# Kernel optimization log

Hardware: AMD Instinct MI355X
Metric: run time of the kernel (lower is better)

## Reference

```python
import jax, jax.numpy as jnp
import numpy as np

B, T, M, P = 512, 64, 256, 256


def setup_inputs() -> dict:
    key = jax.random.key(0)
    ks = jax.random.split(key, 17)
    w = lambda i, shape: (jax.random.normal(ks[i], shape, jnp.float32) * 0.05)
    return {
        "encoded_inputs": jax.random.normal(ks[0], (B, T, M), jnp.float32),
        "y": jax.random.normal(ks[1], (B, T, 1), jnp.float32),
        "tar": jax.random.normal(ks[2], (B, 2), jnp.float32),
        "train": 1,
        "Wd_w": w(3, (M, 2 * P)), "Wd_b": w(4, (M,)),
        "Ud_w": w(5, (M, M)),
        "vd_w": w(6, (1, M)),
        "wt_w": w(7, (1, M + 1)), "wt_b": w(8, (1,)),
        "Wy_w": w(9, (P, P + M)), "Wy_b": w(10, (P,)),
        "vy_w": w(11, (1, P)), "vy_b": w(12, (1,)),
        "Wih": w(13, (4 * P, 1)), "Whh": w(14, (4 * P, P)),
        "bih": w(15, (4 * P,)), "bhh": w(16, (4 * P,)),
    }


def _lstm_cell(x, h, c, Wih, Whh, bih, bhh):
    # torch.nn.LSTMCell gate order: i, f, g, o
    g = x @ Wih.T + h @ Whh.T + (bih + bhh)
    i, f, gg, o = jnp.split(g, 4, axis=1)
    c = jax.nn.sigmoid(f) * c + jax.nn.sigmoid(i) * jnp.tanh(gg)
    h = jax.nn.sigmoid(o) * jnp.tanh(c)
    return h, c


def reference(encoded_inputs, y, tar, train,
              Wd_w, Wd_b, Ud_w, vd_w, wt_w, wt_b,
              Wy_w, Wy_b, vy_w, vy_b, Wih, Whh, bih, bhh):
    Bn = encoded_inputs.shape[0]
    Pn = Whh.shape[1]
    Mn = encoded_inputs.shape[2]
    h0 = jnp.zeros((Bn, Pn), encoded_inputs.dtype)
    c0 = jnp.zeros((Bn, Pn), encoded_inputs.dtype)
    ctx0 = jnp.zeros((Bn, Mn), encoded_inputs.dtype)
    # U_d(encoded_inputs) is loop-invariant
    y1 = jnp.einsum('btm,nm->btn', encoded_inputs, Ud_w)  # (B,T,M)

    def attend(h, s):
        x1 = jnp.concatenate([h, s], axis=1) @ Wd_w.T + Wd_b      # (B,M)
        z1 = jnp.tanh(x1[:, None, :] + y1)                        # (B,T,M)
        l = jnp.einsum('btm,m->bt', z1, vd_w[0])                  # (B,T)
        beta = jax.nn.softmax(l, axis=1)
        return jnp.einsum('bt,btm->bm', beta, encoded_inputs)     # (B,M)

    def step(carry, y_t):
        h, s, _ = carry
        c_t = attend(h, s)
        y_til = jnp.concatenate([c_t, y_t], axis=1) @ wt_w.T + wt_b  # (B,1)
        h, s = _lstm_cell(y_til, h, s, Wih, Whh, bih, bhh)
        return (h, s, c_t), None

    (h, s, c_t), _ = jax.lax.scan(step, (h0, c0, ctx0), jnp.swapaxes(y, 0, 1))

    def head(h):
        return (jnp.concatenate([h, c_t], axis=1) @ Wy_w.T + Wy_b) @ vy_w.T + vy_b

    def extra(h, s, inp):
        y_til = jnp.concatenate([c_t, inp], axis=1) @ wt_w.T + wt_b
        h, s = _lstm_cell(y_til, h, s, Wih, Whh, bih, bhh)
        return h, s, head(h)

    y_Tp1 = head(h)
    if train:
        h, s, y_Tp2 = extra(h, s, tar[:, 0:1])
        h, s, y_Tp3 = extra(h, s, tar[:, 1:2])
    else:
        h, s, y_Tp2 = extra(h, s, y_Tp1)
        h, s, y_Tp3 = extra(h, s, y_Tp2)
    return (y_Tp1, y_Tp2, y_Tp3)
```

## Files before the change

kernel.cpp:

```cpp
#include <hip/hip_runtime.h>


typedef unsigned short u16;
typedef unsigned int u32;
typedef _Float16 half_t;
typedef half_t h2 __attribute__((ext_vector_type(2)));

#define BB 512
#define TT 64
#define MM 256
#define PP 256
#define YS 264
#define ES 68

#define WD16_OFF  0
#define WHH16_OFF 131072
#define WY16_OFF  393216
#define WQ_ELEMS  524288
#define WQ_BYTES  (WQ_ELEMS * 2)

struct H8 { h2 p[4]; };

#if defined(__has_builtin)
#if __has_builtin(__builtin_amdgcn_fdot2)
#define FDOT2(a, b, c) __builtin_amdgcn_fdot2((a), (b), (c), false)
#endif
#endif
#ifndef FDOT2
__device__ __forceinline__ float FDOT2(h2 a, h2 b, float c) {
  return c + (float)a[0] * (float)b[0] + (float)a[1] * (float)b[1];
}
#endif

__device__ __forceinline__ float dot8(const H8 w, const H8 a, float acc) {
  acc = FDOT2(w.p[0], a.p[0], acc);
  acc = FDOT2(w.p[1], a.p[1], acc);
  acc = FDOT2(w.p[2], a.p[2], acc);
  acc = FDOT2(w.p[3], a.p[3], acc);
  return acc;
}
__device__ __forceinline__ u16 f2h(float f) {
  union { half_t h; u16 u; } x; x.h = (half_t)f; return x.u;
}
__device__ __forceinline__ void unpackH8(const H8 v, float f[8]) {
#pragma unroll
  for (int i = 0; i < 8; ++i) f[i] = (float)v.p[i >> 1][i & 1];
}
__device__ __forceinline__ void ldf8(const float* p, float f[8]) {
  float4 a = *(const float4*)p;
  float4 b = *(const float4*)(p + 4);
  f[0]=a.x; f[1]=a.y; f[2]=a.z; f[3]=a.w;
  f[4]=b.x; f[5]=b.y; f[6]=b.z; f[7]=b.w;
}
__device__ __forceinline__ float tanh_fast(float x) {
  float e = __builtin_amdgcn_exp2f(x * 2.885390081777927f);
  return 1.0f - 2.0f * __builtin_amdgcn_rcpf(1.0f + e);
}
__device__ __forceinline__ float sigmoid_fast(float x) {
  float e = __builtin_amdgcn_exp2f(x * -1.4426950408889634f);
  return __builtin_amdgcn_rcpf(1.0f + e);
}

__global__ __launch_bounds__(256) void prep_kernel(
    const float* __restrict__ Wd, const float* __restrict__ Whh,
    const float* __restrict__ Wy, u16* __restrict__ o) {
  int i = blockIdx.x * 256 + threadIdx.x;
  float v;
  if (i < WHH16_OFF) {
    int ki = i & 7, n = (i >> 3) & 255, kb = i >> 11;
    v = Wd[n * 512 + kb * 8 + ki];
  } else if (i < WY16_OFF) {
    int r = i - WHH16_OFF;
    int ki = r & 7, n = (r >> 3) & 1023, kb = r >> 13;
    v = Whh[n * 256 + kb * 8 + ki];
  } else {
    int r = i - WY16_OFF;
    int ki = r & 7, n = (r >> 3) & 255, kb = r >> 11;
    v = Wy[n * 512 + kb * 8 + ki];
  }
  o[i] = f2h(v);
}

template <int WQ>
__global__ __launch_bounds__(256, 2) void scan_kernel(
    const float* __restrict__ E,
    const float* __restrict__ yin,
    const float* __restrict__ tar,
    const int*   __restrict__ train,
    const void*  __restrict__ Wd_q,
    const float* __restrict__ Wd_b,
    const float* __restrict__ Ud_w,
    const float* __restrict__ vd_w,
    const float* __restrict__ wt_w,
    const float* __restrict__ wt_b,
    const void*  __restrict__ Wy_q,
    const float* __restrict__ Wy_b,
    const float* __restrict__ vy_w,
    const float* __restrict__ vy_b,
    const float* __restrict__ Wih,
    const void*  __restrict__ Whh_q,
    const float* __restrict__ bih,
    const float* __restrict__ bhh,
    float* __restrict__ out)
{
  __shared__ __align__(16) u16   y1l[TT * YS];
  __shared__ __align__(16) u16   e16T[MM * ES];
  __shared__ __align__(16) u32   hs16[256];
  __shared__ __align__(16) u32   ctx16p[128];
  __shared__ __align__(16) float ctx[MM];
  __shared__ __align__(16) float x1s[MM];
  __shared__ __align__(16) float lpart[4][TT];
  __shared__ __align__(16) u16   betas16[TT];
  __shared__ float red[4];
  __shared__ float sc[2];

  const int j = threadIdx.x;
  const int b = blockIdx.x;
  const int wv = j >> 6;

  hs16[j] = 0;
  float creg = 0.f;

  {
    const float* __restrict__ Eb = E + (size_t)b * TT * MM;
    for (int i = j; i < TT * MM; i += 256) {
      int t = i >> 8, m = i & 255;
      e16T[m * ES + t] = f2h(Eb[i]);
    }
  }

  {
    const float* __restrict__ Eb = E + (size_t)b * TT * MM;
    const float* __restrict__ Uj = Ud_w + (size_t)j * MM;
    for (int t0 = 0; t0 < TT; t0 += 16) {
      float acc[16];
#pragma unroll
      for (int i = 0; i < 16; ++i) acc[i] = 0.f;
      for (int m0 = 0; m0 < MM; m0 += 8) {
        float w[8]; ldf8(Uj + m0, w);
#pragma unroll
        for (int tt = 0; tt < 16; ++tt) {
          float e[8]; ldf8(Eb + (size_t)(t0 + tt) * MM + m0, e);
#pragma unroll
          for (int mm = 0; mm < 8; ++mm) acc[tt] = fmaf(e[mm], w[mm], acc[tt]);
        }
      }
#pragma unroll
      for (int tt = 0; tt < 16; ++tt)
        y1l[(t0 + tt) * YS + j] = f2h(acc[tt]);
    }
  }
  __syncthreads();

  auto mv4 = [&](float& g0, float& g1, float& g2, float& g3) {
    g0 = g1 = g2 = g3 = 0.f;
    if (WQ) {
      const u16* W = (const u16*)Whh_q;
      const u16* p0 = W + (size_t)j * 8;
      const u16* p1 = p0 + 256 * 8;
      const u16* p2 = p0 + 512 * 8;
      const u16* p3 = p0 + 768 * 8;
#pragma unroll 4
      for (int kb = 0; kb < 32; ++kb) {
        H8 hp = *(const H8*)&hs16[kb * 4];
        g0 = dot8(*(const H8*)p0, hp, g0); p0 += 8192;
        g1 = dot8(*(const H8*)p1, hp, g1); p1 += 8192;
        g2 = dot8(*(const H8*)p2, hp, g2); p2 += 8192;
        g3 = dot8(*(const H8*)p3, hp, g3); p3 += 8192;
      }
    } else {
      const float* W = (const float*)Whh_q;
      const float* p0 = W + (size_t)j * 256;
#pragma unroll 2
      for (int kb = 0; kb < 32; ++kb) {
        H8 hp = *(const H8*)&hs16[kb * 4];
        float hf[8]; unpackH8(hp, hf);
        float w0[8], w1[8], w2[8], w3[8];
        ldf8(p0 + kb * 8, w0);
        ldf8(p0 + 256 * 256 + kb * 8, w1);
        ldf8(p0 + 512 * 256 + kb * 8, w2);
        ldf8(p0 + 768 * 256 + kb * 8, w3);
#pragma unroll
        for (int i = 0; i < 8; ++i) {
          g0 = fmaf(hf[i], w0[i], g0);
          g1 = fmaf(hf[i], w1[i], g1);
          g2 = fmaf(hf[i], w2[i], g2);
          g3 = fmaf(hf[i], w3[i], g3);
        }
      }
    }
  };

  auto gates_apply = [&](float g0, float g1, float g2, float g3, float ytil) {
    g0 += ytil * Wih[j]       + bih[j]       + bhh[j];
    g1 += ytil * Wih[j + 256] + bih[j + 256] + bhh[j + 256];
    g2 += ytil * Wih[j + 512] + bih[j + 512] + bhh[j + 512];
    g3 += ytil * Wih[j + 768] + bih[j + 768] + bhh[j + 768];
    float c = sigmoid_fast(g1) * creg + sigmoid_fast(g0) * tanh_fast(g2);
    float h = sigmoid_fast(g3) * tanh_fast(c);
    creg = c;
    u16* hsu = (u16*)hs16;
    hsu[j] = f2h(h);
    hsu[256 + j] = f2h(c);
  };

  auto head_store = [&](int outIdx) {
    float p = 0.f;
    if (WQ) {
      const u16* W = (const u16*)Wy_q;
      const u16* ph = W + (size_t)j * 8;
      const u16* pc = W + (size_t)(32 * 256 + j) * 8;
#pragma unroll 4
      for (int kb = 0; kb < 32; ++kb) {
        H8 hp = *(const H8*)&hs16[kb * 4];
        H8 cp = *(const H8*)&ctx16p[kb * 4];
        p = dot8(*(const H8*)ph, hp, p); ph += 2048;
        p = dot8(*(const H8*)pc, cp, p); pc += 2048;
      }
    } else {
      const float* W = (const float*)Wy_q + (size_t)j * 512;
      for (int kb = 0; kb < 32; ++kb) {
        H8 hp = *(const H8*)&hs16[kb * 4];
        float hf[8]; unpackH8(hp, hf);
        float w0[8], w1[8];
        ldf8(W + kb * 8, w0);
        ldf8(W + 256 + kb * 8, w1);
#pragma unroll
        for (int i = 0; i < 8; ++i) {
          p = fmaf(hf[i], w0[i], p);
          p = fmaf(ctx[kb * 8 + i], w1[i], p);
        }
      }
    }
    float pp = (p + Wy_b[j]) * vy_w[j];
#pragma unroll
    for (int off = 32; off; off >>= 1) pp += __shfl_xor(pp, off, 64);
    if ((j & 63) == 0) red[wv] = pp;
    __syncthreads();
    if (j == 0) {
      float o = red[0] + red[1] + red[2] + red[3] + vy_b[0];
      out[(size_t)outIdx * BB + b] = o;
      sc[0] = o;
    }
    __syncthreads();
  };

  for (int step = 0; step < TT; ++step) {
    float ax0 = 0.f, ax1 = 0.f, g0, g1, g2, g3;
    {
      if (WQ) {
        const u16* Wd16 = (const u16*)Wd_q;
        const u16* Wh16 = (const u16*)Whh_q;
        const u16* pdh = Wd16 + (size_t)j * 8;
        const u16* pdc = Wd16 + (size_t)(32 * 256 + j) * 8;
        const u16* p0 = Wh16 + (size_t)j * 8;
        const u16* p1 = p0 + 256 * 8;
        const u16* p2 = p0 + 512 * 8;
        const u16* p3 = p0 + 768 * 8;
        float b0 = 0.f, b1 = 0.f, b2 = 0.f, b3 = 0.f;
#pragma unroll 4
        for (int kb = 0; kb < 32; ++kb) {
          H8 hp = *(const H8*)&hs16[kb * 4];
          H8 cp = *(const H8*)&hs16[128 + kb * 4];
          ax0 = dot8(*(const H8*)pdh, hp, ax0); pdh += 2048;
          ax1 = dot8(*(const H8*)pdc, cp, ax1); pdc += 2048;
          b0 = dot8(*(const H8*)p0, hp, b0); p0 += 8192;
          b1 = dot8(*(const H8*)p1, hp, b1); p1 += 8192;
          b2 = dot8(*(const H8*)p2, hp, b2); p2 += 8192;
          b3 = dot8(*(const H8*)p3, hp, b3); p3 += 8192;
        }
        g0 = b0; g1 = b1; g2 = b2; g3 = b3;
      } else {
        const float* wd = (const float*)Wd_q + (size_t)j * 512;
        const float* w0p = (const float*)Whh_q + (size_t)j * 256;
        float b0 = 0.f, b1 = 0.f, b2 = 0.f, b3 = 0.f;
#pragma unroll 2
        for (int kb = 0; kb < 32; ++kb) {
          H8 hp = *(const H8*)&hs16[kb * 4];
          H8 cp = *(const H8*)&hs16[128 + kb * 4];
          float hf[8], cf[8]; unpackH8(hp, hf); unpackH8(cp, cf);
          float wh[8], wc[8], w0[8], w1[8], w2[8], w3[8];
          ldf8(wd + kb * 8, wh);
          ldf8(wd + 256 + kb * 8, wc);
          ldf8(w0p + kb * 8, w0);
          ldf8(w0p + 256 * 256 + kb * 8, w1);
          ldf8(w0p + 512 * 256 + kb * 8, w2);
          ldf8(w0p + 768 * 256 + kb * 8, w3);
#pragma unroll
          for (int i = 0; i < 8; ++i) {
            ax0 = fmaf(hf[i], wh[i], ax0);
            ax1 = fmaf(cf[i], wc[i], ax1);
            b0 = fmaf(hf[i], w0[i], b0);
            b1 = fmaf(hf[i], w1[i], b1);
            b2 = fmaf(hf[i], w2[i], b2);
            b3 = fmaf(hf[i], w3[i], b3);
          }
        }
        g0 = b0; g1 = b1; g2 = b2; g3 = b3;
      }
      x1s[j] = ax0 + ax1 + Wd_b[j];
    }
    __syncthreads();

    {
      const int q = wv, tq = j & 63;
      const u16* __restrict__ yrow = &y1l[tq * YS + q * 64];
      const float* __restrict__ xp = &x1s[q * 64];
      const float* __restrict__ vp = vd_w + q * 64;
      float lp = 0.f;
#pragma unroll 2
      for (int m0 = 0; m0 < 64; m0 += 8) {
        H8 yv = *(const H8*)(yrow + m0);
        float yf[8]; unpackH8(yv, yf);
        float xf[8]; ldf8(xp + m0, xf);
        float vf[8]; ldf8(vp + m0, vf);
#pragma unroll
        for (int mm = 0; mm < 8; ++mm) {
          float z = tanh_fast(xf[mm] + yf[mm]);
          lp = fmaf(z, vf[mm], lp);
        }
      }
      lpart[q][tq] = lp;
    }
    __syncthreads();

    if (j < 64) {
      const int t = j;
      float l = lpart[0][t] + lpart[1][t] + lpart[2][t] + lpart[3][t];
      float mx = l;
#pragma unroll
      for (int off = 32; off; off >>= 1) mx = fmaxf(mx, __shfl_xor(mx, off, 64));
      float e = __builtin_amdgcn_exp2f((l - mx) * 1.4426950408889634f);
      float sm = e;
#pragma unroll
      for (int off = 32; off; off >>= 1) sm += __shfl_xor(sm, off, 64);
      betas16[t] = f2h(e * __builtin_amdgcn_rcpf(sm));
    }
    __syncthreads();

    {
      const u16* __restrict__ ep = &e16T[j * ES];
      float acc = 0.f;
#pragma unroll
      for (int t0 = 0; t0 < TT; t0 += 8) {
        h2 e0 = *(const h2*)(ep + t0);
        h2 e1 = *(const h2*)(ep + t0 + 2);
        h2 e2 = *(const h2*)(ep + t0 + 4);
        h2 e3 = *(const h2*)(ep + t0 + 6);
        H8 bp = *(const H8*)&betas16[t0];
        acc = FDOT2(bp.p[0], e0, acc);
        acc = FDOT2(bp.p[1], e1, acc);
        acc = FDOT2(bp.p[2], e2, acc);
        acc = FDOT2(bp.p[3], e3, acc);
      }
      ctx[j] = acc;
      ((u16*)ctx16p)[j] = f2h(acc);
    }
    {
      float p = ctx[j] * wt_w[j];
#pragma unroll
      for (int off = 32; off; off >>= 1) p += __shfl_xor(p, off, 64);
      if ((j & 63) == 0) red[wv] = p;
    }
    __syncthreads();
    {
      float ytil = red[0] + red[1] + red[2] + red[3]
                 + yin[(size_t)b * TT + step] * wt_w[MM] + wt_b[0];
      gates_apply(g0, g1, g2, g3, ytil);
    }
    __syncthreads();
  }

  float ctdot;
  {
    float p = ctx[j] * wt_w[j];
#pragma unroll
    for (int off = 32; off; off >>= 1) p += __shfl_xor(p, off, 64);
    if ((j & 63) == 0) red[wv] = p;
    __syncthreads();
    ctdot = red[0] + red[1] + red[2] + red[3];
    __syncthreads();
  }

  head_store(0);

  const int tr = train[0];
  for (int e = 0; e < 2; ++e) {
    float inp = tr ? tar[(size_t)b * 2 + e] : sc[0];
    float ytil = ctdot + inp * wt_w[MM] + wt_b[0];
    float g0, g1, g2, g3;
    mv4(g0, g1, g2, g3);
    gates_apply(g0, g1, g2, g3, ytil);
    __syncthreads();
    head_store(1 + e);
  }
}

extern "C" void kernel_launch(void* const* d_in, const int* in_sizes, int n_in,
                              void* d_out, int out_size, void* d_ws, size_t ws_size,
                              hipStream_t stream) {
  const float* E     = (const float*)d_in[0];
  const float* yin   = (const float*)d_in[1];
  const float* tar   = (const float*)d_in[2];
  const int*   train = (const int*)d_in[3];
  const float* Wd_w  = (const float*)d_in[4];
  const float* Wd_b  = (const float*)d_in[5];
  const float* Ud_w  = (const float*)d_in[6];
  const float* vd_w  = (const float*)d_in[7];
  const float* wt_w  = (const float*)d_in[8];
  const float* wt_b  = (const float*)d_in[9];
  const float* Wy_w  = (const float*)d_in[10];
  const float* Wy_b  = (const float*)d_in[11];
  const float* vy_w  = (const float*)d_in[12];
  const float* vy_b  = (const float*)d_in[13];
  const float* Wih   = (const float*)d_in[14];
  const float* Whh   = (const float*)d_in[15];
  const float* bih   = (const float*)d_in[16];
  const float* bhh   = (const float*)d_in[17];

  float* out = (float*)d_out;

  if (ws_size >= (size_t)WQ_BYTES) {
    u16* wq = (u16*)d_ws;
    prep_kernel<<<dim3(WQ_ELEMS / 256), dim3(256), 0, stream>>>(
        Wd_w, Whh, Wy_w, wq);
    scan_kernel<1><<<dim3(BB), dim3(256), 0, stream>>>(
        E, yin, tar, train, wq + WD16_OFF, Wd_b, Ud_w, vd_w, wt_w, wt_b,
        wq + WY16_OFF, Wy_b, vy_w, vy_b, Wih, wq + WHH16_OFF, bih, bhh, out);
  } else {
    scan_kernel<0><<<dim3(BB), dim3(256), 0, stream>>>(
        E, yin, tar, train, Wd_w, Wd_b, Ud_w, vd_w, wt_w, wt_b,
        Wy_w, Wy_b, vy_w, vy_b, Wih, Whh, bih, bhh, out);
  }

  (void)in_sizes; (void)n_in; (void)out_size;
}
```

Measured before the change: 1.192 ms.

## Process two batch rows per block with split-K matvecs sharing weight loads

Each block now handles two batch rows with 512 threads. The two thread halves split the K dimension of the recurrent and attention matvecs, and each weight vector load is reused for both rows, with partial sums combined through shared memory. The intent is to halve per-row weight traffic from global/L2 and double the work per block. The cost is doubled LDS use per block (two copies of y1 and E^T), which likely limits occupancy to one block per CU, plus extra reduction syncs.

```diff
diff --git a/kernel.cpp b/kernel.cpp
--- a/kernel.cpp
+++ b/kernel.cpp
@@ -12,6 +12,8 @@
 #define PP 256
 #define YS 264
 #define ES 68
+#define NROW 2
+#define NTH 512
 
 #define WD16_OFF  0
 #define WHH16_OFF 131072
@@ -82,7 +84,7 @@
 }
 
 template <int WQ>
-__global__ __launch_bounds__(256, 2) void scan_kernel(
+__global__ __launch_bounds__(NTH, 2) void scan_kernel(
     const float* __restrict__ E,
     const float* __restrict__ yin,
     const float* __restrict__ tar,
@@ -103,35 +105,49 @@
     const float* __restrict__ bhh,
     float* __restrict__ out)
 {
-  __shared__ __align__(16) u16   y1l[TT * YS];
-  __shared__ __align__(16) u16   e16T[MM * ES];
-  __shared__ __align__(16) u32   hs16[256];
-  __shared__ __align__(16) u32   ctx16p[128];
-  __shared__ __align__(16) float ctx[MM];
-  __shared__ __align__(16) float x1s[MM];
-  __shared__ __align__(16) float lpart[4][TT];
-  __shared__ __align__(16) u16   betas16[TT];
-  __shared__ float red[4];
-  __shared__ float sc[2];
-
-  const int j = threadIdx.x;
-  const int b = blockIdx.x;
+  __shared__ __align__(16) u16   y1l[NROW][TT * YS];
+  __shared__ __align__(16) u16   e16T[NROW][MM * ES];
+  __shared__ __align__(16) u32   hs16[NROW][256];
+  __shared__ __align__(16) u32   ctx16p[NROW][128];
+  __shared__ __align__(16) float ctx[NROW][MM];
+  __shared__ __align__(16) float x1a[NROW][MM];
+  __shared__ __align__(16) float x1b[NROW][MM];
+  __shared__ __align__(16) float lpart[NROW][4][TT];
+  __shared__ __align__(16) u16   betas16[NROW][TT];
+  __shared__ __align__(16) float part[10][MM];
+  __shared__ float red[8];
+  __shared__ float sc[NROW];
+
+  const int j  = threadIdx.x;
+  const int n  = j & 255;
+  const int kh = j >> 8;
   const int wv = j >> 6;
-
-  hs16[j] = 0;
-  float creg = 0.f;
+  const int b0 = blockIdx.x * NROW;
+
+  ((u32*)hs16)[j] = 0;
+  float creg0 = 0.f, creg1 = 0.f;
+
+  const float wih0 = Wih[n],       wih1 = Wih[n + 256];
+  const float wih2 = Wih[n + 512], wih3 = Wih[n + 768];
+  const float bb0 = bih[n]       + bhh[n];
+  const float bb1 = bih[n + 256] + bhh[n + 256];
+  const float bb2 = bih[n + 512] + bhh[n + 512];
+  const float bb3 = bih[n + 768] + bhh[n + 768];
+  const float wtM = wt_w[MM], wtb = wt_b[0];
 
   {
-    const float* __restrict__ Eb = E + (size_t)b * TT * MM;
-    for (int i = j; i < TT * MM; i += 256) {
-      int t = i >> 8, m = i & 255;
-      e16T[m * ES + t] = f2h(Eb[i]);
+    const float* __restrict__ Eb0 = E + (size_t)b0 * TT * MM;
+    for (int i = j; i < NROW * TT * MM; i += NTH) {
+      int r = i >> 14;
+      int idx = i & 16383;
+      int t = idx >> 8, m = idx & 255;
+      e16T[r][m * ES + t] = f2h(Eb0[i]);
     }
   }
 
   {
-    const float* __restrict__ Eb = E + (size_t)b * TT * MM;
-    const float* __restrict__ Uj = Ud_w + (size_t)j * MM;
+    const float* __restrict__ Eb = E + (size_t)(b0 + kh) * TT * MM;
+    const float* __restrict__ Uj = Ud_w + (size_t)n * MM;
     for (int t0 = 0; t0 < TT; t0 += 16) {
       float acc[16];
 #pragma unroll
@@ -147,186 +163,202 @@
       }
 #pragma unroll
       for (int tt = 0; tt < 16; ++tt)
-        y1l[(t0 + tt) * YS + j] = f2h(acc[tt]);
+        y1l[kh][(t0 + tt) * YS + n] = f2h(acc[tt]);
     }
   }
   __syncthreads();
 
-  auto mv4 = [&](float& g0, float& g1, float& g2, float& g3) {
-    g0 = g1 = g2 = g3 = 0.f;
+  auto gates_apply = [&](int r, float g0, float g1, float g2, float g3,
+                         float ytil) {
+    g0 += ytil * wih0 + bb0;
+    g1 += ytil * wih1 + bb1;
+    g2 += ytil * wih2 + bb2;
+    g3 += ytil * wih3 + bb3;
+    float& cr = r ? creg1 : creg0;
+    float c = sigmoid_fast(g1) * cr + sigmoid_fast(g0) * tanh_fast(g2);
+    float h = sigmoid_fast(g3) * tanh_fast(c);
+    cr = c;
+    u16* hsu = (u16*)hs16[r];
+    hsu[n] = f2h(h);
+    hsu[256 + n] = f2h(c);
+  };
+
+  auto head_store = [&](int outIdx) {
+    float p0 = 0.f, p1 = 0.f;
     if (WQ) {
-      const u16* W = (const u16*)Whh_q;
-      const u16* p0 = W + (size_t)j * 8;
-      const u16* p1 = p0 + 256 * 8;
-      const u16* p2 = p0 + 512 * 8;
-      const u16* p3 = p0 + 768 * 8;
+      const u16* Wy16 = (const u16*)Wy_q;
+      const u16* ph = Wy16 + (size_t)((kh * 16) * 256 + n) * 8;
+      const u16* pc = Wy16 + (size_t)((32 + kh * 16) * 256 + n) * 8;
+      const u32* hb0 = &hs16[0][kh * 64];
+      const u32* hb1 = &hs16[1][kh * 64];
+      const u32* cb0 = &ctx16p[0][kh * 64];
+      const u32* cb1 = &ctx16p[1][kh * 64];
 #pragma unroll 4
-      for (int kb = 0; kb < 32; ++kb) {
-        H8 hp = *(const H8*)&hs16[kb * 4];
-        g0 = dot8(*(const H8*)p0, hp, g0); p0 += 8192;
-        g1 = dot8(*(const H8*)p1, hp, g1); p1 += 8192;
-        g2 = dot8(*(const H8*)p2, hp, g2); p2 += 8192;
-        g3 = dot8(*(const H8*)p3, hp, g3); p3 += 8192;
+      for (int kb2 = 0; kb2 < 16; ++kb2) {
+        H8 wh = *(const H8*)ph; ph += 2048;
+        H8 wc = *(const H8*)pc; pc += 2048;
+        H8 hp0 = *(const H8*)&hb0[kb2 * 4];
+        H8 hp1 = *(const H8*)&hb1[kb2 * 4];
+        H8 cp0 = *(const H8*)&cb0[kb2 * 4];
+        H8 cp1 = *(const H8*)&cb1[kb2 * 4];
+        p0 = dot8(wh, hp0, p0); p0 = dot8(wc, cp0, p0);
+        p1 = dot8(wh, hp1, p1); p1 = dot8(wc, cp1, p1);
       }
     } else {
-      const float* W = (const float*)Whh_q;
-      const float* p0 = W + (size_t)j * 256;
+      const float* W = (const float*)Wy_q + (size_t)n * 512 + kh * 128;
 #pragma unroll 2
-      for (int kb = 0; kb < 32; ++kb) {
-        H8 hp = *(const H8*)&hs16[kb * 4];
-        float hf[8]; unpackH8(hp, hf);
-        float w0[8], w1[8], w2[8], w3[8];
-        ldf8(p0 + kb * 8, w0);
-        ldf8(p0 + 256 * 256 + kb * 8, w1);
-        ldf8(p0 + 512 * 256 + kb * 8, w2);
-        ldf8(p0 + 768 * 256 + kb * 8, w3);
+      for (int kb2 = 0; kb2 < 16; ++kb2) {
+        H8 hp0v = *(const H8*)&hs16[0][kh * 64 + kb2 * 4];
+        H8 hp1v = *(const H8*)&hs16[1][kh * 64 + kb2 * 4];
+        float hf0[8], hf1[8]; unpackH8(hp0v, hf0); unpackH8(hp1v, hf1);
+        float ch0[8], ch1[8];
+        ldf8(&ctx[0][kh * 128 + kb2 * 8], ch0);
+        ldf8(&ctx[1][kh * 128 + kb2 * 8], ch1);
+        float wh[8], wc[8];
+        ldf8(W + kb2 * 8, wh);
+        ldf8(W + 256 + kb2 * 8, wc);
 #pragma unroll
         for (int i = 0; i < 8; ++i) {
-          g0 = fmaf(hf[i], w0[i], g0);
-          g1 = fmaf(hf[i], w1[i], g1);
-          g2 = fmaf(hf[i], w2[i], g2);
-          g3 = fmaf(hf[i], w3[i], g3);
+          p0 = fmaf(hf0[i], wh[i], p0); p0 = fmaf(ch0[i], wc[i], p0);
+          p1 = fmaf(hf1[i], wh[i], p1); p1 = fmaf(ch1[i], wc[i], p1);
         }
       }
     }
+    if (kh) { part[0][n] = p0; part[1][n] = p1; }
+    __syncthreads();
+    if (kh == 0) {
+      float q0 = (p0 + part[0][n] + Wy_b[n]) * vy_w[n];
+      float q1 = (p1 + part[1][n] + Wy_b[n]) * vy_w[n];
+#pragma unroll
+      for (int off = 32; off; off >>= 1) {
+        q0 += __shfl_xor(q0, off, 64);
+        q1 += __shfl_xor(q1, off, 64);
+      }
+      if ((j & 63) == 0) { red[wv] = q0; red[4 + wv] = q1; }
+    }
+    __syncthreads();
+    if (j == 0) {
+      float o0 = red[0] + red[1] + red[2] + red[3] + vy_b[0];
+      float o1 = red[4] + red[5] + red[6] + red[7] + vy_b[0];
+      out[(size_t)outIdx * BB + b0] = o0;
+      out[(size_t)outIdx * BB + b0 + 1] = o1;
+      sc[0] = o0; sc[1] = o1;
+    }
+    __syncthreads();
   };
 
-  auto gates_apply = [&](float g0, float g1, float g2, float g3, float ytil) {
-    g0 += ytil * Wih[j]       + bih[j]       + bhh[j];
-    g1 += ytil * Wih[j + 256] + bih[j + 256] + bhh[j + 256];
-    g2 += ytil * Wih[j + 512] + bih[j + 512] + bhh[j + 512];
-    g3 += ytil * Wih[j + 768] + bih[j + 768] + bhh[j + 768];
-    float c = sigmoid_fast(g1) * creg + sigmoid_fast(g0) * tanh_fast(g2);
-    float h = sigmoid_fast(g3) * tanh_fast(c);
-    creg = c;
-    u16* hsu = (u16*)hs16;
-    hsu[j] = f2h(h);
-    hsu[256 + j] = f2h(c);
-  };
-
-  auto head_store = [&](int outIdx) {
-    float p = 0.f;
-    if (WQ) {
-      const u16* W = (const u16*)Wy_q;
-      const u16* ph = W + (size_t)j * 8;
-      const u16* pc = W + (size_t)(32 * 256 + j) * 8;
-#pragma unroll 4
-      for (int kb = 0; kb < 32; ++kb) {
-        H8 hp = *(const H8*)&hs16[kb * 4];
-        H8 cp = *(const H8*)&ctx16p[kb * 4];
-        p = dot8(*(const H8*)ph, hp, p); ph += 2048;
-        p = dot8(*(const H8*)pc, cp, p); pc += 2048;
-      }
-    } else {
-      const float* W = (const float*)Wy_q + (size_t)j * 512;
-      for (int kb = 0; kb < 32; ++kb) {
-        H8 hp = *(const H8*)&hs16[kb * 4];
-        float hf[8]; unpackH8(hp, hf);
-        float w0[8], w1[8];
-        ldf8(W + kb * 8, w0);
-        ldf8(W + 256 + kb * 8, w1);
-#pragma unroll
-        for (int i = 0; i < 8; ++i) {
-          p = fmaf(hf[i], w0[i], p);
-          p = fmaf(ctx[kb * 8 + i], w1[i], p);
-        }
-      }
-    }
-    float pp = (p + Wy_b[j]) * vy_w[j];
-#pragma unroll
-    for (int off = 32; off; off >>= 1) pp += __shfl_xor(pp, off, 64);
-    if ((j & 63) == 0) red[wv] = pp;
-    __syncthreads();
-    if (j == 0) {
-      float o = red[0] + red[1] + red[2] + red[3] + vy_b[0];
-      out[(size_t)outIdx * BB + b] = o;
-      sc[0] = o;
-    }
-    __syncthreads();
-  };
-
   for (int step = 0; step < TT; ++step) {
-    float ax0 = 0.f, ax1 = 0.f, g0, g1, g2, g3;
+    float sg0r0 = 0, sg0r1 = 0, sg1r0 = 0, sg1r1 = 0;
+    float sg2r0 = 0, sg2r1 = 0, sg3r0 = 0, sg3r1 = 0;
     {
+      float ax0 = 0.f, ax1 = 0.f;
+      float g00 = 0, g01 = 0, g10 = 0, g11 = 0;
+      float g20 = 0, g21 = 0, g30 = 0, g31 = 0;
       if (WQ) {
         const u16* Wd16 = (const u16*)Wd_q;
         const u16* Wh16 = (const u16*)Whh_q;
-        const u16* pdh = Wd16 + (size_t)j * 8;
-        const u16* pdc = Wd16 + (size_t)(32 * 256 + j) * 8;
-        const u16* p0 = Wh16 + (size_t)j * 8;
+        const u16* pdh = Wd16 + (size_t)((kh * 16) * 256 + n) * 8;
+        const u16* pdc = Wd16 + (size_t)((32 + kh * 16) * 256 + n) * 8;
+        const u16* p0 = Wh16 + (size_t)((kh * 16) * 1024 + n) * 8;
         const u16* p1 = p0 + 256 * 8;
         const u16* p2 = p0 + 512 * 8;
         const u16* p3 = p0 + 768 * 8;
-        float b0 = 0.f, b1 = 0.f, b2 = 0.f, b3 = 0.f;
+        const u32* hb0 = &hs16[0][kh * 64];
+        const u32* hb1 = &hs16[1][kh * 64];
+        const u32* cb0 = &hs16[0][128 + kh * 64];
+        const u32* cb1 = &hs16[1][128 + kh * 64];
 #pragma unroll 4
-        for (int kb = 0; kb < 32; ++kb) {
-          H8 hp = *(const H8*)&hs16[kb * 4];
-          H8 cp = *(const H8*)&hs16[128 + kb * 4];
-          ax0 = dot8(*(const H8*)pdh, hp, ax0); pdh += 2048;
-          ax1 = dot8(*(const H8*)pdc, cp, ax1); pdc += 2048;
-          b0 = dot8(*(const H8*)p0, hp, b0); p0 += 8192;
-          b1 = dot8(*(const H8*)p1, hp, b1); p1 += 8192;
-          b2 = dot8(*(const H8*)p2, hp, b2); p2 += 8192;
-          b3 = dot8(*(const H8*)p3, hp, b3); p3 += 8192;
+        for (int kb2 = 0; kb2 < 16; ++kb2) {
+          H8 hp0 = *(const H8*)&hb0[kb2 * 4];
+          H8 hp1 = *(const H8*)&hb1[kb2 * 4];
+          H8 cp0 = *(const H8*)&cb0[kb2 * 4];
+          H8 cp1 = *(const H8*)&cb1[kb2 * 4];
+          H8 wdh = *(const H8*)pdh; pdh += 2048;
+          H8 wdc = *(const H8*)pdc; pdc += 2048;
+          H8 w0 = *(const H8*)p0; p0 += 8192;
+          H8 w1 = *(const H8*)p1; p1 += 8192;
+          H8 w2 = *(const H8*)p2; p2 += 8192;
+          H8 w3 = *(const H8*)p3; p3 += 8192;
+          ax0 = dot8(wdh, hp0, ax0); ax0 = dot8(wdc, cp0, ax0);
+          ax1 = dot8(wdh, hp1, ax1); ax1 = dot8(wdc, cp1, ax1);
+          g00 = dot8(w0, hp0, g00); g01 = dot8(w0, hp1, g01);
+          g10 = dot8(w1, hp0, g10); g11 = dot8(w1, hp1, g11);
+          g20 = dot8(w2, hp0, g20); g21 = dot8(w2, hp1, g21);
+          g30 = dot8(w3, hp0, g30); g31 = dot8(w3, hp1, g31);
         }
-        g0 = b0; g1 = b1; g2 = b2; g3 = b3;
       } else {
-        const float* wd = (const float*)Wd_q + (size_t)j * 512;
-        const float* w0p = (const float*)Whh_q + (size_t)j * 256;
-        float b0 = 0.f, b1 = 0.f, b2 = 0.f, b3 = 0.f;
+        const float* wdp = (const float*)Wd_q + (size_t)n * 512 + kh * 128;
+        const float* w0p = (const float*)Whh_q + (size_t)n * 256 + kh * 128;
 #pragma unroll 2
-        for (int kb = 0; kb < 32; ++kb) {
-          H8 hp = *(const H8*)&hs16[kb * 4];
-          H8 cp = *(const H8*)&hs16[128 + kb * 4];
-          float hf[8], cf[8]; unpackH8(hp, hf); unpackH8(cp, cf);
+        for (int kb2 = 0; kb2 < 16; ++kb2) {
+          H8 hp0v = *(const H8*)&hs16[0][kh * 64 + kb2 * 4];
+          H8 hp1v = *(const H8*)&hs16[1][kh * 64 + kb2 * 4];
+          H8 cp0v = *(const H8*)&hs16[0][128 + kh * 64 + kb2 * 4];
+          H8 cp1v = *(const H8*)&hs16[1][128 + kh * 64 + kb2 * 4];
+          float hf0[8], hf1[8], cf0[8], cf1[8];
+          unpackH8(hp0v, hf0); unpackH8(hp1v, hf1);
+          unpackH8(cp0v, cf0); unpackH8(cp1v, cf1);
           float wh[8], wc[8], w0[8], w1[8], w2[8], w3[8];
-          ldf8(wd + kb * 8, wh);
-          ldf8(wd + 256 + kb * 8, wc);
-          ldf8(w0p + kb * 8, w0);
-          ldf8(w0p + 256 * 256 + kb * 8, w1);
-          ldf8(w0p + 512 * 256 + kb * 8, w2);
-          ldf8(w0p + 768 * 256 + kb * 8, w3);
+          ldf8(wdp + kb2 * 8, wh);
+          ldf8(wdp + 256 + kb2 * 8, wc);
+          ldf8(w0p + kb2 * 8, w0);
+          ldf8(w0p + 256 * 256 + kb2 * 8, w1);
+          ldf8(w0p + 512 * 256 + kb2 * 8, w2);
+          ldf8(w0p + 768 * 256 + kb2 * 8, w3);
 #pragma unroll
           for (int i = 0; i < 8; ++i) {
-            ax0 = fmaf(hf[i], wh[i], ax0);
-            ax1 = fmaf(cf[i], wc[i], ax1);
-            b0 = fmaf(hf[i], w0[i], b0);
-            b1 = fmaf(hf[i], w1[i], b1);
-            b2 = fmaf(hf[i], w2[i], b2);
-            b3 = fmaf(hf[i], w3[i], b3);
+            ax0 = fmaf(hf0[i], wh[i], ax0); ax0 = fmaf(cf0[i], wc[i], ax0);
+            ax1 = fmaf(hf1[i], wh[i], ax1); ax1 = fmaf(cf1[i], wc[i], ax1);
+            g00 = fmaf(hf0[i], w0[i], g00); g01 = fmaf(hf1[i], w0[i], g01);
+            g10 = fmaf(hf0[i], w1[i], g10); g11 = fmaf(hf1[i], w1[i], g11);
+            g20 = fmaf(hf0[i], w2[i], g20); g21 = fmaf(hf1[i], w2[i], g21);
+            g30 = fmaf(hf0[i], w3[i], g30); g31 = fmaf(hf1[i], w3[i], g31);
           }
         }
-        g0 = b0; g1 = b1; g2 = b2; g3 = b3;
-      }
-      x1s[j] = ax0 + ax1 + Wd_b[j];
+      }
+      if (kh) {
+        x1b[0][n] = ax0; x1b[1][n] = ax1;
+        part[2][n] = g00; part[3][n] = g01;
+        part[4][n] = g10; part[5][n] = g11;
+        part[6][n] = g20; part[7][n] = g21;
+        part[8][n] = g30; part[9][n] = g31;
+      } else {
+        float bia = Wd_b[n];
+        x1a[0][n] = ax0 + bia; x1a[1][n] = ax1 + bia;
+        sg0r0 = g00; sg0r1 = g01; sg1r0 = g10; sg1r1 = g11;
+        sg2r0 = g20; sg2r1 = g21; sg3r0 = g30; sg3r1 = g31;
+      }
     }
     __syncthreads();
 
     {
-      const int q = wv, tq = j & 63;
-      const u16* __restrict__ yrow = &y1l[tq * YS + q * 64];
-      const float* __restrict__ xp = &x1s[q * 64];
+      const int q = (j >> 6) & 3, tq = j & 63;
+      const u16* __restrict__ yrow = &y1l[kh][tq * YS + q * 64];
+      const float* __restrict__ xap = &x1a[kh][q * 64];
+      const float* __restrict__ xbp = &x1b[kh][q * 64];
       const float* __restrict__ vp = vd_w + q * 64;
       float lp = 0.f;
 #pragma unroll 2
       for (int m0 = 0; m0 < 64; m0 += 8) {
         H8 yv = *(const H8*)(yrow + m0);
         float yf[8]; unpackH8(yv, yf);
-        float xf[8]; ldf8(xp + m0, xf);
+        float xf[8]; ldf8(xap + m0, xf);
+        float xg[8]; ldf8(xbp + m0, xg);
         float vf[8]; ldf8(vp + m0, vf);
 #pragma unroll
         for (int mm = 0; mm < 8; ++mm) {
-          float z = tanh_fast(xf[mm] + yf[mm]);
+          float z = tanh_fast(xf[mm] + xg[mm] + yf[mm]);
           lp = fmaf(z, vf[mm], lp);
         }
       }
-      lpart[q][tq] = lp;
-    }
-    __syncthreads();
-
-    if (j < 64) {
-      const int t = j;
-      float l = lpart[0][t] + lpart[1][t] + lpart[2][t] + lpart[3][t];
+      lpart[kh][q][tq] = lp;
+    }
+    __syncthreads();
+
+    if (n < 64) {
+      const int t = n;
+      float l = lpart[kh][0][t] + lpart[kh][1][t] + lpart[kh][2][t] +
+                lpart[kh][3][t];
       float mx = l;
 #pragma unroll
       for (int off = 32; off; off >>= 1) mx = fmaxf(mx, __shfl_xor(mx, off, 64));
@@ -334,12 +366,12 @@
       float sm = e;
 #pragma unroll
       for (int off = 32; off; off >>= 1) sm += __shfl_xor(sm, off, 64);
-      betas16[t] = f2h(e * __builtin_amdgcn_rcpf(sm));
+      betas16[kh][t] = f2h(e * __builtin_amdgcn_rcpf(sm));
     }
     __syncthreads();
 
     {
-      const u16* __restrict__ ep = &e16T[j * ES];
+      const u16* __restrict__ ep = &e16T[kh][n * ES];
       float acc = 0.f;
 #pragma unroll
       for (int t0 = 0; t0 < TT; t0 += 8) {
@@ -347,50 +379,109 @@
         h2 e1 = *(const h2*)(ep + t0 + 2);
         h2 e2 = *(const h2*)(ep + t0 + 4);
         h2 e3 = *(const h2*)(ep + t0 + 6);
-        H8 bp = *(const H8*)&betas16[t0];
+        H8 bp = *(const H8*)&betas16[kh][t0];
         acc = FDOT2(bp.p[0], e0, acc);
         acc = FDOT2(bp.p[1], e1, acc);
         acc = FDOT2(bp.p[2], e2, acc);
         acc = FDOT2(bp.p[3], e3, acc);
       }
-      ctx[j] = acc;
-      ((u16*)ctx16p)[j] = f2h(acc);
-    }
-    {
-      float p = ctx[j] * wt_w[j];
+      ctx[kh][n] = acc;
+      ((u16*)ctx16p[kh])[n] = f2h(acc);
+      float p = acc * wt_w[n];
 #pragma unroll
       for (int off = 32; off; off >>= 1) p += __shfl_xor(p, off, 64);
       if ((j & 63) == 0) red[wv] = p;
     }
     __syncthreads();
-    {
-      float ytil = red[0] + red[1] + red[2] + red[3]
-                 + yin[(size_t)b * TT + step] * wt_w[MM] + wt_b[0];
-      gates_apply(g0, g1, g2, g3, ytil);
-    }
-    __syncthreads();
-  }
-
-  float ctdot;
+
+    if (kh == 0) {
+      float yt0 = red[0] + red[1] + red[2] + red[3] +
+                  yin[(size_t)b0 * TT + step] * wtM + wtb;
+      float yt1 = red[4] + red[5] + red[6] + red[7] +
+                  yin[(size_t)(b0 + 1) * TT + step] * wtM + wtb;
+      gates_apply(0, sg0r0 + part[2][n], sg1r0 + part[4][n],
+                  sg2r0 + part[6][n], sg3r0 + part[8][n], yt0);
+      gates_apply(1, sg0r1 + part[3][n], sg1r1 + part[5][n],
+                  sg2r1 + part[7][n], sg3r1 + part[9][n], yt1);
+    }
+    __syncthreads();
+  }
+
   {
-    float p = ctx[j] * wt_w[j];
+    float p = ctx[kh][n] * wt_w[n];
 #pragma unroll
     for (int off = 32; off; off >>= 1) p += __shfl_xor(p, off, 64);
     if ((j & 63) == 0) red[wv] = p;
-    __syncthreads();
-    ctdot = red[0] + red[1] + red[2] + red[3];
-    __syncthreads();
-  }
+  }
+  __syncthreads();
+  const float ctdot0 = red[0] + red[1] + red[2] + red[3];
+  const float ctdot1 = red[4] + red[5] + red[6] + red[7];
 
   head_store(0);
 
   const int tr = train[0];
   for (int e = 0; e < 2; ++e) {
-    float inp = tr ? tar[(size_t)b * 2 + e] : sc[0];
-    float ytil = ctdot + inp * wt_w[MM] + wt_b[0];
-    float g0, g1, g2, g3;
-    mv4(g0, g1, g2, g3);
-    gates_apply(g0, g1, g2, g3, ytil);
+    float g00 = 0, g01 = 0, g10 = 0, g11 = 0;
+    float g20 = 0, g21 = 0, g30 = 0, g31 = 0;
+    if (WQ) {
+      const u16* Wh16 = (const u16*)Whh_q;
+      const u16* p0 = Wh16 + (size_t)((kh * 16) * 1024 + n) * 8;
+      const u16* p1 = p0 + 256 * 8;
+      const u16* p2 = p0 + 512 * 8;
+      const u16* p3 = p0 + 768 * 8;
+      const u32* hb0 = &hs16[0][kh * 64];
+      const u32* hb1 = &hs16[1][kh * 64];
+#pragma unroll 4
+      for (int kb2 = 0; kb2 < 16; ++kb2) {
+        H8 hp0 = *(const H8*)&hb0[kb2 * 4];
+        H8 hp1 = *(const H8*)&hb1[kb2 * 4];
+        H8 w0 = *(const H8*)p0; p0 += 8192;
+        H8 w1 = *(const H8*)p1; p1 += 8192;
+        H8 w2 = *(const H8*)p2; p2 += 8192;
+        H8 w3 = *(const H8*)p3; p3 += 8192;
+        g00 = dot8(w0, hp0, g00); g01 = dot8(w0, hp1, g01);
+        g10 = dot8(w1, hp0, g10); g11 = dot8(w1, hp1, g11);
+        g20 = dot8(w2, hp0, g20); g21 = dot8(w2, hp1, g21);
+        g30 = dot8(w3, hp0, g30); g31 = dot8(w3, hp1, g31);
+      }
+    } else {
+      const float* w0p = (const float*)Whh_q + (size_t)n * 256 + kh * 128;
+#pragma unroll 2
+      for (int kb2 = 0; kb2 < 16; ++kb2) {
+        H8 hp0v = *(const H8*)&hs16[0][kh * 64 + kb2 * 4];
+        H8 hp1v = *(const H8*)&hs16[1][kh * 64 + kb2 * 4];
+        float hf0[8], hf1[8]; unpackH8(hp0v, hf0); unpackH8(hp1v, hf1);
+        float w0[8], w1[8], w2[8], w3[8];
+        ldf8(w0p + kb2 * 8, w0);
+        ldf8(w0p + 256 * 256 + kb2 * 8, w1);
+        ldf8(w0p + 512 * 256 + kb2 * 8, w2);
+        ldf8(w0p + 768 * 256 + kb2 * 8, w3);
+#pragma unroll
+        for (int i = 0; i < 8; ++i) {
+          g00 = fmaf(hf0[i], w0[i], g00); g01 = fmaf(hf1[i], w0[i], g01);
+          g10 = fmaf(hf0[i], w1[i], g10); g11 = fmaf(hf1[i], w1[i], g11);
+          g20 = fmaf(hf0[i], w2[i], g20); g21 = fmaf(hf1[i], w2[i], g21);
+          g30 = fmaf(hf0[i], w3[i], g30); g31 = fmaf(hf1[i], w3[i], g31);
+        }
+      }
+    }
+    if (kh) {
+      part[2][n] = g00; part[3][n] = g01;
+      part[4][n] = g10; part[5][n] = g11;
+      part[6][n] = g20; part[7][n] = g21;
+      part[8][n] = g30; part[9][n] = g31;
+    }
+    __syncthreads();
+    if (kh == 0) {
+      float inp0 = tr ? tar[(size_t)b0 * 2 + e] : sc[0];
+      float inp1 = tr ? tar[(size_t)(b0 + 1) * 2 + e] : sc[1];
+      float yt0 = ctdot0 + inp0 * wtM + wtb;
+      float yt1 = ctdot1 + inp1 * wtM + wtb;
+      gates_apply(0, g00 + part[2][n], g10 + part[4][n],
+                  g20 + part[6][n], g30 + part[8][n], yt0);
+      gates_apply(1, g01 + part[3][n], g11 + part[5][n],
+                  g21 + part[7][n], g31 + part[9][n], yt1);
+    }
     __syncthreads();
     head_store(1 + e);
   }
@@ -424,11 +515,11 @@
     u16* wq = (u16*)d_ws;
     prep_kernel<<<dim3(WQ_ELEMS / 256), dim3(256), 0, stream>>>(
         Wd_w, Whh, Wy_w, wq);
-    scan_kernel<1><<<dim3(BB), dim3(256), 0, stream>>>(
+    scan_kernel<1><<<dim3(BB / NROW), dim3(NTH), 0, stream>>>(
         E, yin, tar, train, wq + WD16_OFF, Wd_b, Ud_w, vd_w, wt_w, wt_b,
         wq + WY16_OFF, Wy_b, vy_w, vy_b, Wih, wq + WHH16_OFF, bih, bhh, out);
   } else {
-    scan_kernel<0><<<dim3(BB), dim3(256), 0, stream>>>(
+    scan_kernel<0><<<dim3(BB / NROW), dim3(NTH), 0, stream>>>(
         E, yin, tar, train, Wd_w, Wd_b, Ud_w, vd_w, wt_w, wt_b,
         Wy_w, Wy_b, vy_w, vy_b, Wih, Whh, bih, bhh, out);
   }
```

New measurement: 1.101 ms. -7.7%, faster.
